# Kernel tuning notes

Measured on AMD Instinct MI355X. Metric: run time of the kernel, lower is better.

Reference implementation:

```python
import jax, jax.numpy as jnp
import numpy as np

BN_EPS = 1e-5


def _bn(h, gamma, beta, mean, var):
    return (h - mean) * jax.lax.rsqrt(var + BN_EPS) * gamma + beta


def _gin_conv(x, edge_index, edge_weight, Wa, ba, g, be, m, v, Wb, bb):
    # GINConv: (1+eps)*x + sum_j w_ij * x_j, eps=0; then MLP: Linear->BN->ReLU->Linear
    src, dst = edge_index[0], edge_index[1]
    msg = x[src] * edge_weight[:, None]                      # [E, C]
    agg = jax.ops.segment_sum(msg, dst, num_segments=x.shape[0])  # [N, C]
    h = x + agg
    h = h @ Wa + ba
    h = jax.nn.relu(_bn(h, g, be, m, v))
    return h @ Wb + bb


def setup_inputs() -> dict:
    key = jax.random.key(0)
    ks = jax.random.split(key, 16)
    N, E, C_IN, C_OUT, H = 100000, 1600000, 128, 64, 32
    x = jax.random.normal(ks[0], (N, C_IN), dtype=jnp.float32)
    edge_index = jax.random.randint(ks[1], (2, E), 0, N, dtype=jnp.int32)
    edge_weight = jax.random.uniform(ks[2], (E,), dtype=jnp.float32)
    s1 = 1.0 / np.sqrt(C_IN)
    s2 = 1.0 / np.sqrt(H)
    return {
        "x": x,
        "edge_weight": edge_weight,
        "W1a": jax.random.normal(ks[3], (C_IN, H), dtype=jnp.float32) * s1,
        "b1a": jnp.zeros((H,), jnp.float32),
        "g1": jnp.ones((H,), jnp.float32),
        "be1": jnp.zeros((H,), jnp.float32),
        "m1": jax.random.normal(ks[4], (H,), dtype=jnp.float32) * 0.1,
        "v1": jax.random.uniform(ks[5], (H,), dtype=jnp.float32) + 0.5,
        "W1b": jax.random.normal(ks[6], (H, H), dtype=jnp.float32) * s2,
        "b1b": jnp.zeros((H,), jnp.float32),
        "W2a": jax.random.normal(ks[7], (H, C_OUT), dtype=jnp.float32) * s2,
        "b2a": jnp.zeros((C_OUT,), jnp.float32),
        "g2": jnp.ones((C_OUT,), jnp.float32),
        "be2": jnp.zeros((C_OUT,), jnp.float32),
        "m2": jax.random.normal(ks[8], (C_OUT,), dtype=jnp.float32) * 0.1,
        "v2": jax.random.uniform(ks[9], (C_OUT,), dtype=jnp.float32) + 0.5,
        "W2b": jax.random.normal(ks[10], (C_OUT, C_OUT), dtype=jnp.float32) * (1.0 / np.sqrt(C_OUT)),
        "b2b": jnp.zeros((C_OUT,), jnp.float32),
        "edge_index": edge_index,
    }


def reference(x, edge_weight, W1a, b1a, g1, be1, m1, v1, W1b, b1b,
              W2a, b2a, g2, be2, m2, v2, W2b, b2b, edge_index):
    # eval mode: dropout(p=0.6) is identity, BN uses running stats
    h = jax.nn.relu(_gin_conv(x, edge_index, edge_weight,
                              W1a, b1a, g1, be1, m1, v1, W1b, b1b))
    out = _gin_conv(h, edge_index, edge_weight,
                    W2a, b2a, g2, be2, m2, v2, W2b, b2b)
    return out
```

## Files before the change

### kernel.cpp

```cpp
#include <hip/hip_runtime.h>


#define BN_EPS 1e-5f
#define BKT 128
#define BKT_SH 7
#define EPB 4096
#define MAXB 800

__device__ __forceinline__ unsigned short f2bf(float f) {
    unsigned u = __float_as_uint(f);
    return (unsigned short)((u + 0x7FFFu + ((u >> 16) & 1u)) >> 16);
}
__device__ __forceinline__ float bf2f(unsigned short b) {
    return __uint_as_float(((unsigned)b) << 16);
}
__device__ __forceinline__ float bflo(unsigned u) { return __uint_as_float(u << 16); }
__device__ __forceinline__ float bfhi(unsigned u) { return __uint_as_float(u & 0xFFFF0000u); }

__device__ __forceinline__ void gacc8(uint4 v, float w, float* acc) {
    acc[0] += bflo(v.x) * w; acc[1] += bfhi(v.x) * w;
    acc[2] += bflo(v.y) * w; acc[3] += bfhi(v.y) * w;
    acc[4] += bflo(v.z) * w; acc[5] += bfhi(v.z) * w;
    acc[6] += bflo(v.w) * w; acc[7] += bfhi(v.w) * w;
}

__device__ __forceinline__ void gather_seg8(const unsigned short* __restrict__ tab,
                                            const int2* __restrict__ epack,
                                            int e, int end, int c0, float* acc) {
    long long q0 = 0, q1 = 0, q2 = 0, q3 = 0;
    if (e + 4 <= end) {
        q0 = *(const long long*)&epack[e + 0];
        q1 = *(const long long*)&epack[e + 1];
        q2 = *(const long long*)&epack[e + 2];
        q3 = *(const long long*)&epack[e + 3];
    }
    for (; e + 8 <= end; e += 4) {
        int s0 = (int)(q0 & 0xFFFFF), s1 = (int)(q1 & 0xFFFFF);
        int s2 = (int)(q2 & 0xFFFFF), s3 = (int)(q3 & 0xFFFFF);
        float w0 = __int_as_float((int)(q0 >> 32));
        float w1 = __int_as_float((int)(q1 >> 32));
        float w2 = __int_as_float((int)(q2 >> 32));
        float w3 = __int_as_float((int)(q3 >> 32));
        uint4 v0 = *(const uint4*)&tab[(size_t)s0 * 32 + c0];
        uint4 v1 = *(const uint4*)&tab[(size_t)s1 * 32 + c0];
        uint4 v2 = *(const uint4*)&tab[(size_t)s2 * 32 + c0];
        uint4 v3 = *(const uint4*)&tab[(size_t)s3 * 32 + c0];
        q0 = *(const long long*)&epack[e + 4];
        q1 = *(const long long*)&epack[e + 5];
        q2 = *(const long long*)&epack[e + 6];
        q3 = *(const long long*)&epack[e + 7];
        gacc8(v0, w0, acc); gacc8(v1, w1, acc);
        gacc8(v2, w2, acc); gacc8(v3, w3, acc);
    }
    if (e + 4 <= end) {
        int s0 = (int)(q0 & 0xFFFFF), s1 = (int)(q1 & 0xFFFFF);
        int s2 = (int)(q2 & 0xFFFFF), s3 = (int)(q3 & 0xFFFFF);
        float w0 = __int_as_float((int)(q0 >> 32));
        float w1 = __int_as_float((int)(q1 >> 32));
        float w2 = __int_as_float((int)(q2 >> 32));
        float w3 = __int_as_float((int)(q3 >> 32));
        uint4 v0 = *(const uint4*)&tab[(size_t)s0 * 32 + c0];
        uint4 v1 = *(const uint4*)&tab[(size_t)s1 * 32 + c0];
        uint4 v2 = *(const uint4*)&tab[(size_t)s2 * 32 + c0];
        uint4 v3 = *(const uint4*)&tab[(size_t)s3 * 32 + c0];
        gacc8(v0, w0, acc); gacc8(v1, w1, acc);
        gacc8(v2, w2, acc); gacc8(v3, w3, acc);
        e += 4;
    }
    for (; e < end; ++e) {
        long long q = *(const long long*)&epack[e];
        int sn = (int)(q & 0xFFFFF);
        float w = __int_as_float((int)(q >> 32));
        uint4 v = *(const uint4*)&tab[(size_t)sn * 32 + c0];
        gacc8(v, w, acc);
    }
}

__global__ __launch_bounds__(256) void gemm1_kernel(const float* __restrict__ x,
                                                    const float* __restrict__ W,
                                                    unsigned short* __restrict__ y1b, int N) {
    __shared__ float xs[32][129];
    __shared__ float ws[128 * 32];
    int t = threadIdx.x;
    for (int i = t; i < 4096; i += 256) ws[i] = W[i];
    int row0 = blockIdx.x * 32;
    for (int j = 0; j < 4; ++j) {
        int f4 = t + j * 256;
        int r  = f4 >> 5;
        int kc = (f4 & 31) << 2;
        if (row0 + r < N) {
            float4 v = *(const float4*)&x[(size_t)(row0 + r) * 128 + kc];
            xs[r][kc + 0] = v.x; xs[r][kc + 1] = v.y;
            xs[r][kc + 2] = v.z; xs[r][kc + 3] = v.w;
        }
    }
    __syncthreads();
    int r  = t >> 3;
    int c0 = (t & 7) << 2;
    if (row0 + r >= N) return;
    float a0 = 0.f, a1 = 0.f, a2 = 0.f, a3 = 0.f;
    #pragma unroll 8
    for (int k = 0; k < 128; ++k) {
        float xv = xs[r][k];
        const float* wr = &ws[k * 32 + c0];
        a0 += xv * wr[0]; a1 += xv * wr[1]; a2 += xv * wr[2]; a3 += xv * wr[3];
    }
    ushort4 o = {f2bf(a0), f2bf(a1), f2bf(a2), f2bf(a3)};
    *(ushort4*)&y1b[(size_t)(row0 + r) * 32 + c0] = o;
}

__global__ __launch_bounds__(256) void stage_kernel(const int* __restrict__ ei,
                                                    const float* __restrict__ ew,
                                                    int* __restrict__ gcur,
                                                    int2* __restrict__ staged,
                                                    int E, int cap, int NBUCK) {
    __shared__ int hist[MAXB], base_[MAXB], curs[MAXB], gbase[MAXB];
    __shared__ int2 data[EPB];
    __shared__ unsigned short bslot[EPB];
    int t  = threadIdx.x;
    int e0 = blockIdx.x * EPB;
    int cnt = min(EPB, E - e0);
    for (int i = t; i < MAXB; i += 256) hist[i] = 0;
    __syncthreads();
    for (int i = t; i < cnt; i += 256) {
        int d = ei[(size_t)E + e0 + i];
        atomicAdd(&hist[d >> BKT_SH], 1);
    }
    __syncthreads();
    int lo = t * 4;
    int vb[4];
    int s = 0;
    #pragma unroll
    for (int j = 0; j < 4; ++j) {
        int idx = lo + j;
        vb[j] = (idx < MAXB) ? hist[idx] : 0;
        s += vb[j];
    }
    gbase[t] = s;
    __syncthreads();
    for (int off = 1; off < 256; off <<= 1) {
        int x = (t >= off) ? gbase[t - off] : 0;
        __syncthreads();
        gbase[t] += x;
        __syncthreads();
    }
    int excl = gbase[t] - s;
    #pragma unroll
    for (int j = 0; j < 4; ++j) {
        int idx = lo + j;
        if (idx < MAXB) { base_[idx] = excl; curs[idx] = excl; }
        excl += vb[j];
    }
    __syncthreads();
    for (int i = t; i < cnt; i += 256) {
        int sn = ei[e0 + i];
        int d  = ei[(size_t)E + e0 + i];
        float w = ew[e0 + i];
        int b = d >> BKT_SH, dl = d & (BKT - 1);
        int pos = atomicAdd(&curs[b], 1);
        data[pos]  = make_int2((dl << 20) | sn, __float_as_int(w));
        bslot[pos] = (unsigned short)b;
    }
    __syncthreads();
    for (int b = t; b < NBUCK; b += 256) {
        int c = hist[b];
        gbase[b] = c ? atomicAdd(&gcur[b * 16], c) : 0;
    }
    __syncthreads();
    for (int i = t; i < cnt; i += 256) {
        int b  = bslot[i];
        int gp = gbase[b] + (i - base_[b]);
        if (gp < cap) staged[(size_t)b * cap + gp] = data[i];
    }
}

__global__ __launch_bounds__(1024) void bscan_kernel(const int* __restrict__ gcur,
                                                     int* __restrict__ bbase,
                                                     int* __restrict__ row_ptr_N,
                                                     int NBUCK, int cap) {
    __shared__ int ps[1024];
    int t = threadIdx.x;
    int v = (t < NBUCK) ? min(gcur[t * 16], cap) : 0;
    ps[t] = v;
    __syncthreads();
    for (int off = 1; off < 1024; off <<= 1) {
        int x = (t >= off) ? ps[t - off] : 0;
        __syncthreads();
        ps[t] += x;
        __syncthreads();
    }
    if (t < NBUCK) bbase[t] = ps[t] - v;
    if (t == 1023) *row_ptr_N = ps[1023];
}

__global__ __launch_bounds__(256) void refill_kernel(const int2* __restrict__ staged,
                                                     const int* __restrict__ gcur,
                                                     const int* __restrict__ bbase,
                                                     int2* __restrict__ epack,
                                                     int* __restrict__ row_ptr,
                                                     int N, int cap) {
    __shared__ int hist[BKT];
    __shared__ int curs[BKT];
    int b = blockIdx.x, t = threadIdx.x;
    int cnt  = min(gcur[b * 16], cap);
    int base = bbase[b];
    size_t e0 = (size_t)b * cap;
    if (t < BKT) hist[t] = 0;
    __syncthreads();
    for (int i = t; i < cnt; i += 256) atomicAdd(&hist[staged[e0 + i].x >> 20], 1);
    __syncthreads();
    if (t < BKT) curs[t] = hist[t];
    __syncthreads();
    for (int off = 1; off < BKT; off <<= 1) {
        int y = (t < BKT && t >= off) ? curs[t - off] : 0;
        __syncthreads();
        if (t < BKT) curs[t] += y;
        __syncthreads();
    }
    if (t < BKT) {
        int excl = curs[t] - hist[t];
        int node = (b << BKT_SH) + t;
        if (node < N) row_ptr[node] = base + excl;
        curs[t] = excl;
    }
    __syncthreads();
    for (int i = t; i < cnt; i += 256) {
        int2 p = staged[e0 + i];
        int dl = p.x >> 20;
        int pos = base + atomicAdd(&curs[dl], 1);
        epack[pos] = make_int2(p.x & 0xFFFFF, p.y);
    }
}

__global__ __launch_bounds__(128) void layer1_kernel(
    const unsigned short* __restrict__ y1b, const int* __restrict__ row_ptr,
    const int2* __restrict__ epack,
    const float* __restrict__ b1a, const float* __restrict__ g1,
    const float* __restrict__ be1, const float* __restrict__ m1,
    const float* __restrict__ v1, const float* __restrict__ W1b,
    const float* __restrict__ b1b, unsigned short* __restrict__ h1b, int N) {
    __shared__ float w1b[1024];
    __shared__ float t1s[32][33];
    int t = threadIdx.x;
    for (int i = t; i < 1024; i += 128) w1b[i] = W1b[i];
    int g = t >> 2, l = t & 3;
    int node = blockIdx.x * 32 + g;
    int c0 = l << 3;
    bool act = node < N;
    float acc[8] = {0.f, 0.f, 0.f, 0.f, 0.f, 0.f, 0.f, 0.f};
    if (act) {
        int beg = row_ptr[node];
        int end = row_ptr[node + 1];
        gather_seg8(y1b, epack, beg, end, c0, acc);
        uint4 sv = *(const uint4*)&y1b[(size_t)node * 32 + c0];
        gacc8(sv, 1.f, acc);
        #pragma unroll
        for (int j = 0; j < 8; ++j) {
            int c = c0 + j;
            float scale = g1[c] * rsqrtf(v1[c] + BN_EPS);
            t1s[g][c] = fmaxf((acc[j] + b1a[c] - m1[c]) * scale + be1[c], 0.f);
        }
    }
    __syncthreads();
    if (act) {
        float a[8];
        #pragma unroll
        for (int j = 0; j < 8; ++j) a[j] = b1b[c0 + j];
        #pragma unroll
        for (int k = 0; k < 32; ++k) {
            float tv = t1s[g][k];
            const float* wr = &w1b[k * 32 + c0];
            #pragma unroll
            for (int j = 0; j < 8; ++j) a[j] += tv * wr[j];
        }
        unsigned long long p0 = 0, p1 = 0;
        #pragma unroll
        for (int j = 0; j < 4; ++j)
            p0 |= (unsigned long long)f2bf(fmaxf(a[j], 0.f)) << (16 * j);
        #pragma unroll
        for (int j = 0; j < 4; ++j)
            p1 |= (unsigned long long)f2bf(fmaxf(a[4 + j], 0.f)) << (16 * j);
        __builtin_nontemporal_store(p0, (unsigned long long*)&h1b[(size_t)node * 32 + c0 + 0]);
        __builtin_nontemporal_store(p1, (unsigned long long*)&h1b[(size_t)node * 32 + c0 + 4]);
    }
}

__global__ __launch_bounds__(128) void layer2a_kernel(
    const unsigned short* __restrict__ h1b, const int* __restrict__ row_ptr,
    const int2* __restrict__ epack,
    const float* __restrict__ W2a, const float* __restrict__ b2a,
    const float* __restrict__ g2, const float* __restrict__ be2,
    const float* __restrict__ m2, const float* __restrict__ v2,
    unsigned short* __restrict__ t2b, int N) {
    __shared__ float w2a[2048];
    __shared__ float s1s[32][33];
    __shared__ float sc2s[64], sh2s[64];
    int t = threadIdx.x;
    for (int i = t; i < 2048; i += 128) w2a[i] = W2a[i];
    if (t < 64) {
        float sc = g2[t] * rsqrtf(v2[t] + BN_EPS);
        sc2s[t] = sc;
        sh2s[t] = (b2a[t] - m2[t]) * sc + be2[t];
    }
    int g = t >> 2, l = t & 3;
    int node = blockIdx.x * 32 + g;
    int c0 = l << 3;
    bool act = node < N;
    float acc[8] = {0.f, 0.f, 0.f, 0.f, 0.f, 0.f, 0.f, 0.f};
    if (act) {
        int beg = row_ptr[node];
        int end = row_ptr[node + 1];
        gather_seg8(h1b, epack, beg, end, c0, acc);
        uint4 sv = *(const uint4*)&h1b[(size_t)node * 32 + c0];
        gacc8(sv, 1.f, acc);
        #pragma unroll
        for (int j = 0; j < 8; ++j) s1s[g][c0 + j] = acc[j];
    }
    __syncthreads();
    if (act) {
        int d0 = l << 4;
        float a[16];
        #pragma unroll
        for (int j = 0; j < 16; ++j) a[j] = 0.f;
        #pragma unroll
        for (int k = 0; k < 32; ++k) {
            float sv = s1s[g][k];
            const float* wr = &w2a[k * 64 + d0];
            #pragma unroll
            for (int j = 0; j < 16; ++j) a[j] += sv * wr[j];
        }
        unsigned long long pk[4] = {0, 0, 0, 0};
        #pragma unroll
        for (int j = 0; j < 16; ++j) {
            int c = d0 + j;
            float o = fmaxf(a[j] * sc2s[c] + sh2s[c], 0.f);
            pk[j >> 2] |= (unsigned long long)f2bf(o) << (16 * (j & 3));
        }
        #pragma unroll
        for (int q = 0; q < 4; ++q)
            __builtin_nontemporal_store(pk[q],
                (unsigned long long*)&t2b[(size_t)node * 64 + d0 + 4 * q]);
    }
}

__global__ __launch_bounds__(256) void final_kernel(const unsigned short* __restrict__ t2b,
                                                    const float* __restrict__ W2b,
                                                    const float* __restrict__ b2b,
                                                    float* __restrict__ out, int N) {
    __shared__ float w2b[4096];
    __shared__ float t2s[32][68];
    int t = threadIdx.x;
    for (int i = t; i < 4096; i += 256) w2b[i] = W2b[i];
    int g = t >> 3, l = t & 7;
    int node = blockIdx.x * 32 + g;
    int c0 = l << 3;
    bool act = node < N;
    if (act) {
        uint4 v = *(const uint4*)&t2b[(size_t)node * 64 + c0];
        t2s[g][c0 + 0] = bflo(v.x); t2s[g][c0 + 1] = bfhi(v.x);
        t2s[g][c0 + 2] = bflo(v.y); t2s[g][c0 + 3] = bfhi(v.y);
        t2s[g][c0 + 4] = bflo(v.z); t2s[g][c0 + 5] = bfhi(v.z);
        t2s[g][c0 + 6] = bflo(v.w); t2s[g][c0 + 7] = bfhi(v.w);
    }
    __syncthreads();
    if (act) {
        float a[8];
        #pragma unroll
        for (int j = 0; j < 8; ++j) a[j] = b2b[c0 + j];
        #pragma unroll 8
        for (int k = 0; k < 64; ++k) {
            float tv = t2s[g][k];
            const float* wr = &w2b[k * 64 + c0];
            float4 w0 = *(const float4*)wr;
            float4 w1 = *(const float4*)(wr + 4);
            a[0] += tv * w0.x; a[1] += tv * w0.y; a[2] += tv * w0.z; a[3] += tv * w0.w;
            a[4] += tv * w1.x; a[5] += tv * w1.y; a[6] += tv * w1.z; a[7] += tv * w1.w;
        }
        *(float4*)&out[(size_t)node * 64 + c0 + 0] = *(float4*)&a[0];
        *(float4*)&out[(size_t)node * 64 + c0 + 4] = *(float4*)&a[4];
    }
}

extern "C" void kernel_launch(void* const* d_in, const int* in_sizes, int n_in,
                              void* d_out, int out_size, void* d_ws, size_t ws_size,
                              hipStream_t stream) {
    const float* x   = (const float*)d_in[0];
    const float* ew  = (const float*)d_in[1];
    const float* W1a = (const float*)d_in[2];
    const float* b1a = (const float*)d_in[3];
    const float* g1  = (const float*)d_in[4];
    const float* be1 = (const float*)d_in[5];
    const float* m1  = (const float*)d_in[6];
    const float* v1  = (const float*)d_in[7];
    const float* W1b = (const float*)d_in[8];
    const float* b1b = (const float*)d_in[9];
    const float* W2a = (const float*)d_in[10];
    const float* b2a = (const float*)d_in[11];
    const float* g2  = (const float*)d_in[12];
    const float* be2 = (const float*)d_in[13];
    const float* m2  = (const float*)d_in[14];
    const float* v2  = (const float*)d_in[15];
    const float* W2b = (const float*)d_in[16];
    const float* b2b = (const float*)d_in[17];
    const int*   ei  = (const int*)d_in[18];

    const int N = in_sizes[0] / 128;
    const int E = in_sizes[1];
    const int NBUCK = (N + BKT - 1) >> BKT_SH;

    unsigned short* y1b = (unsigned short*)d_ws;
    int2*  epack   = (int2*)(y1b + (size_t)N * 32);
    int*   row_ptr = (int*)(epack + E);
    int*   gcur    = row_ptr + N + 1;
    int*   bbase   = gcur + (size_t)NBUCK * 16;
    int2*  staged  = (int2*)(bbase + NBUCK + 16);
    unsigned short* h1b = (unsigned short*)staged;
    unsigned short* t2b = h1b + (size_t)N * 32;

    size_t fixed_bytes = (char*)staged - (char*)d_ws;
    size_t avail = (ws_size > fixed_bytes) ? (ws_size - fixed_bytes) : 0;
    int cap = (int)((avail / sizeof(int2)) / NBUCK);
    cap &= ~63;
    if (cap > 2560) cap = 2560;

    hipMemsetAsync(gcur, 0, (size_t)NBUCK * 16 * sizeof(int), stream);

    gemm1_kernel<<<(N + 31) / 32, 256, 0, stream>>>(x, W1a, y1b, N);
    stage_kernel<<<(E + EPB - 1) / EPB, 256, 0, stream>>>(ei, ew, gcur, staged, E, cap, NBUCK);
    bscan_kernel<<<1, 1024, 0, stream>>>(gcur, bbase, &row_ptr[N], NBUCK, cap);
    refill_kernel<<<NBUCK, 256, 0, stream>>>(staged, gcur, bbase, epack, row_ptr, N, cap);
    layer1_kernel<<<(N + 31) / 32, 128, 0, stream>>>(y1b, row_ptr, epack,
                                                     b1a, g1, be1, m1, v1, W1b, b1b, h1b, N);
    layer2a_kernel<<<(N + 31) / 32, 128, 0, stream>>>(h1b, row_ptr, epack,
                                                      W2a, b2a, g2, be2, m2, v2, t2b, N);
    final_kernel<<<(N + 31) / 32, 256, 0, stream>>>(t2b, W2b, b2b, (float*)d_out, N);
}
```

Measured before the change: 181.0 us.

## Drop bucket scan with padded per-bucket CSR, fuse counter reset, cache staged edges in LDS

Removes the single-block bucket scan kernel by giving each bucket a fixed padded region of size cap in the edge array, with per-node (start,end) pairs replacing row_ptr. The gcur reset memset is folded into gemm1, refill caches its staged edges in LDS instead of reading global memory twice, edge-list loads use nontemporal hints, and the gather kernels use 256-thread blocks with 64 nodes each. In exchange the edge array is padded, so workspace use grows and cap may shrink, and edges beyond cap could be dropped.

Result: faster. 172.6 us (-4.6%).

```diff
diff --git a/kernel.cpp b/kernel.cpp
--- a/kernel.cpp
+++ b/kernel.cpp
@@ -6,13 +6,11 @@
 #define BKT_SH 7
 #define EPB 4096
 #define MAXB 800
+#define LDS_E 2560
 
 __device__ __forceinline__ unsigned short f2bf(float f) {
     unsigned u = __float_as_uint(f);
     return (unsigned short)((u + 0x7FFFu + ((u >> 16) & 1u)) >> 16);
-}
-__device__ __forceinline__ float bf2f(unsigned short b) {
-    return __uint_as_float(((unsigned)b) << 16);
 }
 __device__ __forceinline__ float bflo(unsigned u) { return __uint_as_float(u << 16); }
 __device__ __forceinline__ float bfhi(unsigned u) { return __uint_as_float(u & 0xFFFF0000u); }
@@ -29,14 +27,13 @@
                                             int e, int end, int c0, float* acc) {
     long long q0 = 0, q1 = 0, q2 = 0, q3 = 0;
     if (e + 4 <= end) {
-        q0 = *(const long long*)&epack[e + 0];
-        q1 = *(const long long*)&epack[e + 1];
-        q2 = *(const long long*)&epack[e + 2];
-        q3 = *(const long long*)&epack[e + 3];
+        q0 = __builtin_nontemporal_load((const long long*)&epack[e + 0]);
+        q1 = __builtin_nontemporal_load((const long long*)&epack[e + 1]);
+        q2 = __builtin_nontemporal_load((const long long*)&epack[e + 2]);
+        q3 = __builtin_nontemporal_load((const long long*)&epack[e + 3]);
     }
     for (; e + 8 <= end; e += 4) {
-        int s0 = (int)(q0 & 0xFFFFF), s1 = (int)(q1 & 0xFFFFF);
-        int s2 = (int)(q2 & 0xFFFFF), s3 = (int)(q3 & 0xFFFFF);
+        int s0 = (int)q0, s1 = (int)q1, s2 = (int)q2, s3 = (int)q3;
         float w0 = __int_as_float((int)(q0 >> 32));
         float w1 = __int_as_float((int)(q1 >> 32));
         float w2 = __int_as_float((int)(q2 >> 32));
@@ -45,16 +42,15 @@
         uint4 v1 = *(const uint4*)&tab[(size_t)s1 * 32 + c0];
         uint4 v2 = *(const uint4*)&tab[(size_t)s2 * 32 + c0];
         uint4 v3 = *(const uint4*)&tab[(size_t)s3 * 32 + c0];
-        q0 = *(const long long*)&epack[e + 4];
-        q1 = *(const long long*)&epack[e + 5];
-        q2 = *(const long long*)&epack[e + 6];
-        q3 = *(const long long*)&epack[e + 7];
+        q0 = __builtin_nontemporal_load((const long long*)&epack[e + 4]);
+        q1 = __builtin_nontemporal_load((const long long*)&epack[e + 5]);
+        q2 = __builtin_nontemporal_load((const long long*)&epack[e + 6]);
+        q3 = __builtin_nontemporal_load((const long long*)&epack[e + 7]);
         gacc8(v0, w0, acc); gacc8(v1, w1, acc);
         gacc8(v2, w2, acc); gacc8(v3, w3, acc);
     }
     if (e + 4 <= end) {
-        int s0 = (int)(q0 & 0xFFFFF), s1 = (int)(q1 & 0xFFFFF);
-        int s2 = (int)(q2 & 0xFFFFF), s3 = (int)(q3 & 0xFFFFF);
+        int s0 = (int)q0, s1 = (int)q1, s2 = (int)q2, s3 = (int)q3;
         float w0 = __int_as_float((int)(q0 >> 32));
         float w1 = __int_as_float((int)(q1 >> 32));
         float w2 = __int_as_float((int)(q2 >> 32));
@@ -68,8 +64,8 @@
         e += 4;
     }
     for (; e < end; ++e) {
-        long long q = *(const long long*)&epack[e];
-        int sn = (int)(q & 0xFFFFF);
+        long long q = __builtin_nontemporal_load((const long long*)&epack[e]);
+        int sn = (int)q;
         float w = __int_as_float((int)(q >> 32));
         uint4 v = *(const uint4*)&tab[(size_t)sn * 32 + c0];
         gacc8(v, w, acc);
@@ -78,10 +74,18 @@
 
 __global__ __launch_bounds__(256) void gemm1_kernel(const float* __restrict__ x,
                                                     const float* __restrict__ W,
-                                                    unsigned short* __restrict__ y1b, int N) {
+                                                    unsigned short* __restrict__ y1b,
+                                                    int* __restrict__ gcur,
+                                                    int N, int ncur) {
     __shared__ float xs[32][129];
     __shared__ float ws[128 * 32];
     int t = threadIdx.x;
+    if (t == 0) {
+        int b0 = blockIdx.x * 8;
+        #pragma unroll
+        for (int j = 0; j < 8; ++j)
+            if (b0 + j < ncur) gcur[b0 + j] = 0;
+    }
     for (int i = t; i < 4096; i += 256) ws[i] = W[i];
     int row0 = blockIdx.x * 32;
     for (int j = 0; j < 4; ++j) {
@@ -174,40 +178,25 @@
     }
 }
 
-__global__ __launch_bounds__(1024) void bscan_kernel(const int* __restrict__ gcur,
-                                                     int* __restrict__ bbase,
-                                                     int* __restrict__ row_ptr_N,
-                                                     int NBUCK, int cap) {
-    __shared__ int ps[1024];
-    int t = threadIdx.x;
-    int v = (t < NBUCK) ? min(gcur[t * 16], cap) : 0;
-    ps[t] = v;
-    __syncthreads();
-    for (int off = 1; off < 1024; off <<= 1) {
-        int x = (t >= off) ? ps[t - off] : 0;
-        __syncthreads();
-        ps[t] += x;
-        __syncthreads();
-    }
-    if (t < NBUCK) bbase[t] = ps[t] - v;
-    if (t == 1023) *row_ptr_N = ps[1023];
-}
-
 __global__ __launch_bounds__(256) void refill_kernel(const int2* __restrict__ staged,
                                                      const int* __restrict__ gcur,
-                                                     const int* __restrict__ bbase,
                                                      int2* __restrict__ epack,
-                                                     int* __restrict__ row_ptr,
+                                                     int2* __restrict__ row_se,
                                                      int N, int cap) {
+    __shared__ int2 ebuf[LDS_E];
     __shared__ int hist[BKT];
     __shared__ int curs[BKT];
     int b = blockIdx.x, t = threadIdx.x;
     int cnt  = min(gcur[b * 16], cap);
-    int base = bbase[b];
+    int base = b * cap;
     size_t e0 = (size_t)b * cap;
     if (t < BKT) hist[t] = 0;
     __syncthreads();
-    for (int i = t; i < cnt; i += 256) atomicAdd(&hist[staged[e0 + i].x >> 20], 1);
+    for (int i = t; i < cnt; i += 256) {
+        int2 p = staged[e0 + i];
+        ebuf[i] = p;
+        atomicAdd(&hist[p.x >> 20], 1);
+    }
     __syncthreads();
     if (t < BKT) curs[t] = hist[t];
     __syncthreads();
@@ -220,38 +209,37 @@
     if (t < BKT) {
         int excl = curs[t] - hist[t];
         int node = (b << BKT_SH) + t;
-        if (node < N) row_ptr[node] = base + excl;
+        if (node < N) row_se[node] = make_int2(base + excl, base + excl + hist[t]);
         curs[t] = excl;
     }
     __syncthreads();
     for (int i = t; i < cnt; i += 256) {
-        int2 p = staged[e0 + i];
+        int2 p = ebuf[i];
         int dl = p.x >> 20;
         int pos = base + atomicAdd(&curs[dl], 1);
         epack[pos] = make_int2(p.x & 0xFFFFF, p.y);
     }
 }
 
-__global__ __launch_bounds__(128) void layer1_kernel(
-    const unsigned short* __restrict__ y1b, const int* __restrict__ row_ptr,
+__global__ __launch_bounds__(256) void layer1_kernel(
+    const unsigned short* __restrict__ y1b, const int2* __restrict__ row_se,
     const int2* __restrict__ epack,
     const float* __restrict__ b1a, const float* __restrict__ g1,
     const float* __restrict__ be1, const float* __restrict__ m1,
     const float* __restrict__ v1, const float* __restrict__ W1b,
     const float* __restrict__ b1b, unsigned short* __restrict__ h1b, int N) {
     __shared__ float w1b[1024];
-    __shared__ float t1s[32][33];
+    __shared__ float t1s[64][33];
     int t = threadIdx.x;
-    for (int i = t; i < 1024; i += 128) w1b[i] = W1b[i];
+    for (int i = t; i < 1024; i += 256) w1b[i] = W1b[i];
     int g = t >> 2, l = t & 3;
-    int node = blockIdx.x * 32 + g;
+    int node = blockIdx.x * 64 + g;
     int c0 = l << 3;
     bool act = node < N;
     float acc[8] = {0.f, 0.f, 0.f, 0.f, 0.f, 0.f, 0.f, 0.f};
     if (act) {
-        int beg = row_ptr[node];
-        int end = row_ptr[node + 1];
-        gather_seg8(y1b, epack, beg, end, c0, acc);
+        int2 se = row_se[node];
+        gather_seg8(y1b, epack, se.x, se.y, c0, acc);
         uint4 sv = *(const uint4*)&y1b[(size_t)node * 32 + c0];
         gacc8(sv, 1.f, acc);
         #pragma unroll
@@ -285,32 +273,31 @@
     }
 }
 
-__global__ __launch_bounds__(128) void layer2a_kernel(
-    const unsigned short* __restrict__ h1b, const int* __restrict__ row_ptr,
+__global__ __launch_bounds__(256) void layer2a_kernel(
+    const unsigned short* __restrict__ h1b, const int2* __restrict__ row_se,
     const int2* __restrict__ epack,
     const float* __restrict__ W2a, const float* __restrict__ b2a,
     const float* __restrict__ g2, const float* __restrict__ be2,
     const float* __restrict__ m2, const float* __restrict__ v2,
     unsigned short* __restrict__ t2b, int N) {
     __shared__ float w2a[2048];
-    __shared__ float s1s[32][33];
+    __shared__ float s1s[64][33];
     __shared__ float sc2s[64], sh2s[64];
     int t = threadIdx.x;
-    for (int i = t; i < 2048; i += 128) w2a[i] = W2a[i];
+    for (int i = t; i < 2048; i += 256) w2a[i] = W2a[i];
     if (t < 64) {
         float sc = g2[t] * rsqrtf(v2[t] + BN_EPS);
         sc2s[t] = sc;
         sh2s[t] = (b2a[t] - m2[t]) * sc + be2[t];
     }
     int g = t >> 2, l = t & 3;
-    int node = blockIdx.x * 32 + g;
+    int node = blockIdx.x * 64 + g;
     int c0 = l << 3;
     bool act = node < N;
     float acc[8] = {0.f, 0.f, 0.f, 0.f, 0.f, 0.f, 0.f, 0.f};
     if (act) {
-        int beg = row_ptr[node];
-        int end = row_ptr[node + 1];
-        gather_seg8(h1b, epack, beg, end, c0, acc);
+        int2 se = row_se[node];
+        gather_seg8(h1b, epack, se.x, se.y, c0, acc);
         uint4 sv = *(const uint4*)&h1b[(size_t)node * 32 + c0];
         gacc8(sv, 1.f, acc);
         #pragma unroll
@@ -407,31 +394,27 @@
     const int N = in_sizes[0] / 128;
     const int E = in_sizes[1];
     const int NBUCK = (N + BKT - 1) >> BKT_SH;
+    const int NCUR  = NBUCK * 16;
 
     unsigned short* y1b = (unsigned short*)d_ws;
-    int2*  epack   = (int2*)(y1b + (size_t)N * 32);
-    int*   row_ptr = (int*)(epack + E);
-    int*   gcur    = row_ptr + N + 1;
-    int*   bbase   = gcur + (size_t)NBUCK * 16;
-    int2*  staged  = (int2*)(bbase + NBUCK + 16);
+    int2*  row_se  = (int2*)(y1b + (size_t)N * 32);
+    int*   gcur    = (int*)(row_se + N);
+    int2*  epack   = (int2*)(gcur + NCUR + 16);
+    size_t fixed_bytes = (char*)epack - (char*)d_ws;
+    size_t avail = (ws_size > fixed_bytes) ? (ws_size - fixed_bytes) : 0;
+    int cap = (int)((avail / (2 * sizeof(int2))) / NBUCK);
+    cap &= ~63;
+    if (cap > LDS_E) cap = LDS_E;
+    int2* staged = epack + (size_t)NBUCK * cap;
     unsigned short* h1b = (unsigned short*)staged;
     unsigned short* t2b = h1b + (size_t)N * 32;
 
-    size_t fixed_bytes = (char*)staged - (char*)d_ws;
-    size_t avail = (ws_size > fixed_bytes) ? (ws_size - fixed_bytes) : 0;
-    int cap = (int)((avail / sizeof(int2)) / NBUCK);
-    cap &= ~63;
-    if (cap > 2560) cap = 2560;
-
-    hipMemsetAsync(gcur, 0, (size_t)NBUCK * 16 * sizeof(int), stream);
-
-    gemm1_kernel<<<(N + 31) / 32, 256, 0, stream>>>(x, W1a, y1b, N);
+    gemm1_kernel<<<(N + 31) / 32, 256, 0, stream>>>(x, W1a, y1b, gcur, N, NCUR);
     stage_kernel<<<(E + EPB - 1) / EPB, 256, 0, stream>>>(ei, ew, gcur, staged, E, cap, NBUCK);
-    bscan_kernel<<<1, 1024, 0, stream>>>(gcur, bbase, &row_ptr[N], NBUCK, cap);
-    refill_kernel<<<NBUCK, 256, 0, stream>>>(staged, gcur, bbase, epack, row_ptr, N, cap);
-    layer1_kernel<<<(N + 31) / 32, 128, 0, stream>>>(y1b, row_ptr, epack,
+    refill_kernel<<<NBUCK, 256, 0, stream>>>(staged, gcur, epack, row_se, N, cap);
+    layer1_kernel<<<(N + 63) / 64, 256, 0, stream>>>(y1b, row_se, epack,
                                                      b1a, g1, be1, m1, v1, W1b, b1b, h1b, N);
-    layer2a_kernel<<<(N + 31) / 32, 128, 0, stream>>>(h1b, row_ptr, epack,
+    layer2a_kernel<<<(N + 63) / 64, 256, 0, stream>>>(h1b, row_se, epack,
                                                       W2a, b2a, g2, be2, m2, v2, t2b, N);
     final_kernel<<<(N + 31) / 32, 256, 0, stream>>>(t2b, W2b, b2b, (float*)d_out, N);
 }
```
